# Optimization experiments

Measured on AMD Instinct MI355X. Metric: run time of the kernel, lower is better.

Reference implementation:

```python
import jax, jax.numpy as jnp
import numpy as np

MAX_DISP = 192

def _conv(x, w, b=None, stride=1, pad=0):
    y = jax.lax.conv_general_dilated(x, w, (stride, stride), [(pad, pad), (pad, pad)],
                                     dimension_numbers=('NCHW', 'OIHW', 'NCHW'))
    return y if b is None else y + b[None, :, None, None]

def _inorm(x):  # InstanceNorm2d, affine=False
    m = x.mean((2, 3), keepdims=True)
    v = x.var((2, 3), keepdims=True)
    return (x - m) * jax.lax.rsqrt(v + 1e-5)

def _bnorm(x):  # BatchNorm2d at init (gamma=1, beta=0), batch stats
    m = x.mean((0, 2, 3), keepdims=True)
    v = x.var((0, 2, 3), keepdims=True)
    return (x - m) * jax.lax.rsqrt(v + 1e-5)

def _encoder(x, w1, b1, w2, b2, w3, b3, norm):
    # simplified BasicEncoder: two stride-2 convs -> 1/4 resolution, then 1x1 proj
    x = jax.nn.relu(norm(_conv(x, w1, b1, 2, 3)))
    x = jax.nn.relu(norm(_conv(x, w2, b2, 2, 1)))
    return _conv(x, w3, b3, 1, 0)

def _forward(image1, image2, fnet_w1, fnet_b1, fnet_w2, fnet_b2, fnet_w3, fnet_b3,
             cnet_w1, cnet_b1, cnet_w2, cnet_b2, cnet_w3, cnet_b3,
             bform_a, bform_b, bform_cd_w, bform_cd_b,
             gru_wz, gru_bz, gru_wr, gru_br, gru_wq, gru_bq,
             disp_w1, disp_b1, disp_w2, disp_b2):
    i1 = 2.0 * (image1 / 255.0) - 1.0
    i2 = 2.0 * (image2 / 255.0) - 1.0
    fmap1 = _encoder(i1, fnet_w1, fnet_b1, fnet_w2, fnet_b2, fnet_w3, fnet_b3, _inorm)
    fmap2 = _encoder(i2, fnet_w1, fnet_b1, fnet_w2, fnet_b2, fnet_w3, fnet_b3, _inorm)
    hidden = jnp.tanh(_encoder(i1, cnet_w1, cnet_b1, cnet_w2, cnet_b2, cnet_w3, cnet_b3, _bnorm))
    Wf = fmap1.shape[3]
    for d in range(MAX_DISP // 4):  # 48 sequential width-sweep steps, shrinking overlap
        f1 = fmap1[:, :, :, d:]
        f2 = fmap2[:, :, :, :Wf - d] if d > 0 else fmap2
        # BilinearForm: a(x) + b(y) + cd(x*y), all 1x1 convs
        feat = _conv(f1, bform_a) + _conv(f2, bform_b) + _conv(f1 * f2, bform_cd_w, bform_cd_b)
        h = hidden[:, :, :, d:]
        # gru_input = cat(h, feat); ConvGRU cats hidden again -> [h, h, feat] = 96 ch
        hx = jnp.concatenate([h, h, feat], axis=1)
        z = jax.nn.sigmoid(_conv(hx, gru_wz, gru_bz, 1, 1))
        r = jax.nn.sigmoid(_conv(hx, gru_wr, gru_br, 1, 1))
        q = jnp.tanh(_conv(jnp.concatenate([r * h, h, feat], axis=1), gru_wq, gru_bq, 1, 1))
        h = (1.0 - z) * h + z * q
        hidden = hidden.at[:, :, :, d:].set(h)  # in-place scatter back
    # DisparityHead: conv3x3 -> relu -> conv3x3, negated
    return -_conv(jax.nn.relu(_conv(hidden, disp_w1, disp_b1, 1, 1)), disp_w2, disp_b2, 1, 1)

def setup_inputs():
    key = jax.random.key(0)
    ks = jax.random.split(key, 16)
    B, H, W, D = 1, 384, 640, 32
    def n(k, shape, scale=0.05):
        return (jax.random.normal(k, shape) * scale).astype(jnp.float32)
    z = lambda c: jnp.zeros((c,), jnp.float32)
    return {
        'image1': jax.random.uniform(ks[0], (B, 3, H, W), jnp.float32) * 255.0,
        'image2': jax.random.uniform(ks[1], (B, 3, H, W), jnp.float32) * 255.0,
        'fnet_w1': n(ks[2], (D, 3, 7, 7)), 'fnet_b1': z(D),
        'fnet_w2': n(ks[3], (D, D, 3, 3)), 'fnet_b2': z(D),
        'fnet_w3': n(ks[4], (D, D, 1, 1)), 'fnet_b3': z(D),
        'cnet_w1': n(ks[5], (D, 3, 7, 7)), 'cnet_b1': z(D),
        'cnet_w2': n(ks[6], (D, D, 3, 3)), 'cnet_b2': z(D),
        'cnet_w3': n(ks[7], (D, D, 1, 1)), 'cnet_b3': z(D),
        'bform_a': n(ks[8], (D, D, 1, 1)), 'bform_b': n(ks[9], (D, D, 1, 1)),
        'bform_cd_w': n(ks[10], (D, D, 1, 1)), 'bform_cd_b': z(D),
        'gru_wz': n(ks[11], (D, 3 * D, 3, 3)), 'gru_bz': z(D),
        'gru_wr': n(ks[12], (D, 3 * D, 3, 3)), 'gru_br': z(D),
        'gru_wq': n(ks[13], (D, 3 * D, 3, 3)), 'gru_bq': z(D),
        'disp_w1': n(ks[14], (64, D, 3, 3)), 'disp_b1': z(64),
        'disp_w2': n(ks[15], (1, 64, 3, 3)), 'disp_b2': z(1),
    }

def reference(image1, image2, fnet_w1, fnet_b1, fnet_w2, fnet_b2, fnet_w3, fnet_b3,
              cnet_w1, cnet_b1, cnet_w2, cnet_b2, cnet_w3, cnet_b3,
              bform_a, bform_b, bform_cd_w, bform_cd_b,
              gru_wz, gru_bz, gru_wr, gru_br, gru_wq, gru_bq,
              disp_w1, disp_b1, disp_w2, disp_b2):
    return _forward(image1, image2, fnet_w1, fnet_b1, fnet_w2, fnet_b2, fnet_w3, fnet_b3,
                    cnet_w1, cnet_b1, cnet_w2, cnet_b2, cnet_w3, cnet_b3,
                    bform_a, bform_b, bform_cd_w, bform_cd_b,
                    gru_wz, gru_bz, gru_wr, gru_br, gru_wq, gru_bq,
                    disp_w1, disp_b1, disp_w2, disp_b2)
```

## Files before the change

### kernel.cpp

```cpp
#include <hip/hip_runtime.h>
#include <math.h>

#define H0 384
#define W0 640
#define H1 192
#define W1 320
#define H2 96
#define W2 160
#define NP1 (H1*W1)
#define NP2 (H2*W2)
#define ND  48
#define NBLK2 (NP2/256)
#define CHW ((size_t)32*NP2)
#define PW 162
#define PH 98
#define PSL (PH*PW)
#define PCHW ((size_t)32*PSL)

typedef float v2f __attribute__((ext_vector_type(2)));


__global__ void zero_buf_kernel(float* __restrict__ p, size_t n) {
    size_t i = (size_t)blockIdx.x*256 + threadIdx.x;
    size_t stride = (size_t)gridDim.x*256;
    for (; i < n; i += stride) p[i] = 0.f;
}

__device__ __forceinline__ void twr_dev(const float* __restrict__ in, float* __restrict__ out,
                                        int idx, int CI, int K, int CO) {
    int co = idx % CO;
    int t  = idx / CO;
    int k  = t % K;
    int ci = t / K;
    out[idx] = in[(co*CI + ci)*K + k];
}

__global__ void prep_all(const float* __restrict__ fnet_w1, const float* __restrict__ cnet_w1,
                         const float* __restrict__ fnet_w2, const float* __restrict__ cnet_w2,
                         const float* __restrict__ fnet_w3, const float* __restrict__ cnet_w3,
                         const float* __restrict__ bform_a, const float* __restrict__ bform_b,
                         const float* __restrict__ bform_cd_w, const float* __restrict__ disp_w1,
                         const float* __restrict__ gru_wz, const float* __restrict__ gru_wr,
                         const float* __restrict__ gru_wq,
                         float* __restrict__ we1f, float* __restrict__ we1c,
                         float* __restrict__ we2f, float* __restrict__ we2c,
                         float* __restrict__ w3f, float* __restrict__ w3c,
                         float* __restrict__ wat, float* __restrict__ wbt,
                         float* __restrict__ wct, float* __restrict__ wd1t,
                         float4* __restrict__ wzrpk, float2* __restrict__ wqpk,
                         float* __restrict__ stats) {
    int i = blockIdx.x*256 + threadIdx.x;
    if (i < 4704) { twr_dev(fnet_w1, we1f, i, 3, 49, 32); return; }
    i -= 4704;
    if (i < 4704) { twr_dev(cnet_w1, we1c, i, 3, 49, 32); return; }
    i -= 4704;
    if (i < 9216) { twr_dev(fnet_w2, we2f, i, 32, 9, 32); return; }
    i -= 9216;
    if (i < 9216) { twr_dev(cnet_w2, we2c, i, 32, 9, 32); return; }
    i -= 9216;
    if (i < 1024) { twr_dev(fnet_w3, w3f, i, 32, 1, 32); return; }
    i -= 1024;
    if (i < 1024) { twr_dev(cnet_w3, w3c, i, 32, 1, 32); return; }
    i -= 1024;
    if (i < 1024) { twr_dev(bform_a, wat, i, 32, 1, 32); return; }
    i -= 1024;
    if (i < 1024) { twr_dev(bform_b, wbt, i, 32, 1, 32); return; }
    i -= 1024;
    if (i < 1024) { twr_dev(bform_cd_w, wct, i, 32, 1, 32); return; }
    i -= 1024;
    if (i < 18432) { twr_dev(disp_w1, wd1t, i, 32, 9, 64); return; }
    i -= 18432;
    if (i < 9216) {
        int k  = i % 9;
        int ci = (i/9) % 64;
        int cg = i / (9*64);
        int co0 = cg*2, co1 = co0 + 1;
        float z0, z1, r0, r1;
        if (ci < 32) {
            z0 = gru_wz[(co0*96 + ci)*9 + k] + gru_wz[(co0*96 + ci + 32)*9 + k];
            z1 = gru_wz[(co1*96 + ci)*9 + k] + gru_wz[(co1*96 + ci + 32)*9 + k];
            r0 = gru_wr[(co0*96 + ci)*9 + k] + gru_wr[(co0*96 + ci + 32)*9 + k];
            r1 = gru_wr[(co1*96 + ci)*9 + k] + gru_wr[(co1*96 + ci + 32)*9 + k];
        } else {
            z0 = gru_wz[(co0*96 + ci + 32)*9 + k];
            z1 = gru_wz[(co1*96 + ci + 32)*9 + k];
            r0 = gru_wr[(co0*96 + ci + 32)*9 + k];
            r1 = gru_wr[(co1*96 + ci + 32)*9 + k];
        }
        wzrpk[i] = make_float4(z0, z1, r0, r1);
        return;
    }
    i -= 9216;
    if (i < 13824) {
        int k  = i % 9;
        int ci = (i/9) % 96;
        int cg = i / (9*96);
        wqpk[i] = make_float2(gru_wq[((cg*2)*96 + ci)*9 + k], gru_wq[((cg*2+1)*96 + ci)*9 + k]);
        return;
    }
    i -= 13824;
    if (i < 384) stats[i] = 0.f;
}

__global__ void pad_init_kernel(const float* __restrict__ hidden, float* __restrict__ hwork) {
    int idx = blockIdx.x*256 + threadIdx.x;
    if (idx >= 32*PSL) return;
    int c = idx / PSL;
    int r = idx % PSL;
    int py = r / PW, px = r % PW;
    int y = py - 1, x = px - 1;
    float v = 0.f;
    if ((unsigned)y < (unsigned)H2 && (unsigned)x < (unsigned)W2)
        v = hidden[c*NP2 + y*W2 + x];
    hwork[idx] = v;
}


__global__ void conv7s2_v3(const float* __restrict__ img, const float* __restrict__ wt,
                           const float* __restrict__ b, float* __restrict__ out) {
    int cg = blockIdx.y;
    int co16 = cg*16;
    int sp = blockIdx.x*256 + threadIdx.x;
    int oy = sp / W1, ox = sp % W1;
    float acc[16];
    #pragma unroll
    for (int j = 0; j < 16; ++j) acc[j] = b[co16+j];
    for (int ci = 0; ci < 3; ++ci) {
        for (int ky = 0; ky < 7; ++ky) {
            int iy = 2*oy - 3 + ky;
            if ((unsigned)iy >= (unsigned)H0) continue;
            const float* row  = img + ci*(H0*W0) + iy*W0;
            const float* wrow = wt + (ci*49 + ky*7)*32 + co16;
            #pragma unroll
            for (int kx = 0; kx < 7; ++kx) {
                int ix = 2*ox - 3 + kx;
                if ((unsigned)ix >= (unsigned)W0) continue;
                float v = row[ix]*(2.0f/255.0f) - 1.0f;
                const float4* wp = (const float4*)(wrow + kx*32);
                #pragma unroll
                for (int j4 = 0; j4 < 4; ++j4) {
                    float4 w4 = wp[j4];
                    acc[4*j4+0] += v*w4.x; acc[4*j4+1] += v*w4.y;
                    acc[4*j4+2] += v*w4.z; acc[4*j4+3] += v*w4.w;
                }
            }
        }
    }
    #pragma unroll
    for (int j = 0; j < 16; ++j) out[(co16+j)*NP1 + sp] = acc[j];
}

__global__ void stats_partial_kernel(const float* __restrict__ x, int N, float* __restrict__ st) {
    int c = blockIdx.x >> 3, sl = blockIdx.x & 7;
    int chunk = N >> 3;
    const float4* p = (const float4*)(x + (size_t)c*N + (size_t)sl*chunk);
    int n4 = chunk >> 2;
    float s = 0.f, s2 = 0.f;
    for (int i = threadIdx.x; i < n4; i += 256) {
        float4 v = p[i];
        s  += v.x + v.y + v.z + v.w;
        s2 += v.x*v.x + v.y*v.y + v.z*v.z + v.w*v.w;
    }
    __shared__ float sh1[256], sh2[256];
    sh1[threadIdx.x] = s; sh2[threadIdx.x] = s2;
    __syncthreads();
    for (int o = 128; o > 0; o >>= 1) {
        if (threadIdx.x < o) { sh1[threadIdx.x] += sh1[threadIdx.x+o]; sh2[threadIdx.x] += sh2[threadIdx.x+o]; }
        __syncthreads();
    }
    if (threadIdx.x == 0) { atomicAdd(&st[2*c], sh1[0]); atomicAdd(&st[2*c+1], sh2[0]); }
}

__global__ void norm_relu_v2(float* __restrict__ x, const float* __restrict__ st, int N) {
    int c = blockIdx.y;
    float m    = st[2*c] / (float)N;
    float var  = st[2*c+1] / (float)N - m*m;
    float rstd = rsqrtf(var + 1e-5f);
    float4* p = (float4*)(x + (size_t)c*N);
    int i = blockIdx.x*256 + threadIdx.x;
    float4 v = p[i];
    v.x = fmaxf((v.x-m)*rstd, 0.f); v.y = fmaxf((v.y-m)*rstd, 0.f);
    v.z = fmaxf((v.z-m)*rstd, 0.f); v.w = fmaxf((v.w-m)*rstd, 0.f);
    p[i] = v;
}

__global__ void conv3s2_v2(const float* __restrict__ in, const float* __restrict__ wt,
                           const float* __restrict__ b, float* __restrict__ out) {
    int cg = blockIdx.x / (NP2/256);
    int sp = (blockIdx.x % (NP2/256))*256 + threadIdx.x;
    int co8 = cg*8;
    int oy = sp / W2, ox = sp % W2;
    float acc[8];
    #pragma unroll
    for (int j = 0; j < 8; ++j) acc[j] = b[co8+j];
    for (int ci = 0; ci < 32; ++ci) {
        const float* ip  = in + ci*NP1;
        const float* wci = wt + ci*9*32 + co8;
        #pragma unroll
        for (int ky = 0; ky < 3; ++ky) {
            int iy = 2*oy - 1 + ky;
            if ((unsigned)iy >= (unsigned)H1) continue;
            const float* row = ip + iy*W1;
            #pragma unroll
            for (int kx = 0; kx < 3; ++kx) {
                int ix = 2*ox - 1 + kx;
                if ((unsigned)ix >= (unsigned)W1) continue;
                float v = row[ix];
                const float4* wp = (const float4*)(wci + (ky*3+kx)*32);
                float4 w0 = wp[0], w1 = wp[1];
                acc[0] += v*w0.x; acc[1] += v*w0.y; acc[2] += v*w0.z; acc[3] += v*w0.w;
                acc[4] += v*w1.x; acc[5] += v*w1.y; acc[6] += v*w1.z; acc[7] += v*w1.w;
            }
        }
    }
    #pragma unroll
    for (int j = 0; j < 8; ++j) out[(co8+j)*NP2 + sp] = acc[j];
}

__global__ void conv1x1_v2(const float* __restrict__ in, const float* __restrict__ wt,
                           const float* __restrict__ b, float* __restrict__ out, int mode) {
    int cg = blockIdx.x / (NP2/256);
    int sp = (blockIdx.x % (NP2/256))*256 + threadIdx.x;
    int co8 = cg*8;
    float acc[8];
    #pragma unroll
    for (int j = 0; j < 8; ++j) acc[j] = b[co8+j];
    for (int ci = 0; ci < 32; ++ci) {
        float v = in[ci*NP2 + sp];
        const float4* wp = (const float4*)(wt + ci*32 + co8);
        float4 w0 = wp[0], w1 = wp[1];
        acc[0] += v*w0.x; acc[1] += v*w0.y; acc[2] += v*w0.z; acc[3] += v*w0.w;
        acc[4] += v*w1.x; acc[5] += v*w1.y; acc[6] += v*w1.z; acc[7] += v*w1.w;
    }
    #pragma unroll
    for (int j = 0; j < 8; ++j) {
        float a = acc[j];
        if (mode) a = tanhf(a);
        out[(co8+j)*NP2 + sp] = a;
    }
}


__global__ void feat0_pad_kernel(const float* __restrict__ fmap1, const float* __restrict__ fmap2,
                                 const float* __restrict__ wat, const float* __restrict__ wbt,
                                 const float* __restrict__ wct, const float* __restrict__ bc,
                                 float* __restrict__ featA) {
    int cg  = blockIdx.x / NBLK2;
    int sp  = (blockIdx.x % NBLK2)*256 + threadIdx.x;
    int y = sp / W2;
    int gx = sp % W2;
    int co8 = cg*8;
    float acc[8];
    #pragma unroll
    for (int j = 0; j < 8; ++j) acc[j] = bc[co8+j];
    for (int ci = 0; ci < 32; ++ci) {
        float f1 = fmap1[ci*NP2 + sp];
        float f2 = fmap2[ci*NP2 + sp];
        float f12 = f1*f2;
        const float4* ap = (const float4*)(wat + ci*32 + co8);
        const float4* bp = (const float4*)(wbt + ci*32 + co8);
        const float4* cp = (const float4*)(wct + ci*32 + co8);
        float4 a0 = ap[0], a1 = ap[1];
        float4 b0 = bp[0], b1 = bp[1];
        float4 c0 = cp[0], c1 = cp[1];
        acc[0] += f1*a0.x + f2*b0.x + f12*c0.x;
        acc[1] += f1*a0.y + f2*b0.y + f12*c0.y;
        acc[2] += f1*a0.z + f2*b0.z + f12*c0.z;
        acc[3] += f1*a0.w + f2*b0.w + f12*c0.w;
        acc[4] += f1*a1.x + f2*b1.x + f12*c1.x;
        acc[5] += f1*a1.y + f2*b1.y + f12*c1.y;
        acc[6] += f1*a1.z + f2*b1.z + f12*c1.z;
        acc[7] += f1*a1.w + f2*b1.w + f12*c1.w;
    }
    float* dst = featA + (size_t)(y+1)*PW + (gx+1);
    #pragma unroll
    for (int j = 0; j < 8; ++j) dst[(size_t)(co8+j)*PSL] = acc[j];
}


__global__ __launch_bounds__(256, 4)
void zrf_v6(const float* __restrict__ hworkA, const float* __restrict__ featA,
            const float* __restrict__ fmap1, const float* __restrict__ fmap2,
            const float4* __restrict__ wzrpk,
            const float* __restrict__ wat, const float* __restrict__ wbt,
            const float* __restrict__ wct, const float* __restrict__ bfc,
            const float* __restrict__ bz, const float* __restrict__ br,
            float* __restrict__ zbuf, float* __restrict__ rhpad,
            float* __restrict__ featB, int d, int Wd) {
    __shared__ v2f lwz[64*9], lwr[64*9];
    __shared__ v2f lfa[32], lfb[32], lfc[32];
    int cg  = blockIdx.y;
    int co0 = cg*2;
    {
        const float4* wsrc = wzrpk + (size_t)cg*576;
        for (int i = threadIdx.x; i < 576; i += 256) {
            float4 w = wsrc[i];
            lwz[i] = (v2f){w.x, w.y};
            lwr[i] = (v2f){w.z, w.w};
        }
        if (threadIdx.x < 32) {
            int ci = threadIdx.x;
            lfa[ci] = (v2f){wat[ci*32+co0], wat[ci*32+co0+1]};
            lfb[ci] = (v2f){wbt[ci*32+co0], wbt[ci*32+co0+1]};
            lfc[ci] = (v2f){wct[ci*32+co0], wct[ci*32+co0+1]};
        }
    }
    __syncthreads();
    int sp2 = blockIdx.x*256 + threadIdx.x;
    if (sp2 >= 48*Wd) return;
    int rp = sp2 / Wd;
    int lx = sp2 - rp*Wd;
    int y0 = rp*2;
    int gx = d + lx;
    size_t poff = (size_t)(y0+1)*PW + (gx+1);

    if (lx == 0) {
        #pragma unroll
        for (int j = 0; j < 2; ++j) {
            rhpad[(size_t)(co0+j)*PSL + poff - 1]      = 0.f;
            rhpad[(size_t)(co0+j)*PSL + poff + PW - 1] = 0.f;
        }
    }

    int dn = d + 1;
    if (dn < ND) {
        if (lx == 0) {
            #pragma unroll
            for (int j = 0; j < 2; ++j) {
                featB[(size_t)(co0+j)*PSL + poff]      = 0.f;
                featB[(size_t)(co0+j)*PSL + poff + PW] = 0.f;
            }
        } else {
            v2f f0 = (v2f){bfc[co0], bfc[co0+1]};
            v2f f1 = f0;
            int base1 = y0*W2 + gx;
            #pragma unroll 2
            for (int ci = 0; ci < 32; ++ci) {
                float a1 = fmap1[ci*NP2 + base1];
                float a2 = fmap1[ci*NP2 + base1 + W2];
                float b1 = fmap2[ci*NP2 + base1 - dn];
                float b2 = fmap2[ci*NP2 + base1 + W2 - dn];
                v2f wa = lfa[ci], wb = lfb[ci], wc = lfc[ci];
                f0 += wa*(v2f){a1,a1} + wb*(v2f){b1,b1} + wc*(v2f){a1*b1,a1*b1};
                f1 += wa*(v2f){a2,a2} + wb*(v2f){b2,b2} + wc*(v2f){a2*b2,a2*b2};
            }
            featB[(size_t)co0*PSL + poff]          = f0.x;
            featB[(size_t)(co0+1)*PSL + poff]      = f0.y;
            featB[(size_t)co0*PSL + poff + PW]     = f1.x;
            featB[(size_t)(co0+1)*PSL + poff + PW] = f1.y;
        }
    }

    v2f az0 = (v2f){bz[co0], bz[co0+1]}, az1 = az0;
    v2f ar0 = (v2f){br[co0], br[co0+1]}, ar1 = ar0;
    #pragma unroll
    for (int pass = 0; pass < 2; ++pass) {
        const float* p = (pass == 0 ? hworkA : featA) + poff;
        const v2f* wz = lwz + pass*288;
        const v2f* wr = lwr + pass*288;
        #pragma unroll 2
        for (int ci = 0; ci < 32; ++ci) {
            float v[12];
            #pragma unroll
            for (int r = 0; r < 4; ++r) {
                v[r*3+0] = p[(r-1)*PW - 1];
                v[r*3+1] = p[(r-1)*PW    ];
                v[r*3+2] = p[(r-1)*PW + 1];
            }
            #pragma unroll
            for (int k = 0; k < 9; ++k) {
                int ky = k/3, kx = k - 3*ky;
                float t0 = v[ky*3+kx];
                float t1 = v[(ky+1)*3+kx];
                v2f wzk = wz[k], wrk = wr[k];
                az0 += wzk*(v2f){t0,t0}; az1 += wzk*(v2f){t1,t1};
                ar0 += wrk*(v2f){t0,t0}; ar1 += wrk*(v2f){t1,t1};
            }
            p += PSL;
            wz += 9; wr += 9;
        }
    }
    v2f z0, z1, r0, r1;
    z0.x = 1.f/(1.f + __expf(-az0.x)); z0.y = 1.f/(1.f + __expf(-az0.y));
    z1.x = 1.f/(1.f + __expf(-az1.x)); z1.y = 1.f/(1.f + __expf(-az1.y));
    r0.x = 1.f/(1.f + __expf(-ar0.x)); r0.y = 1.f/(1.f + __expf(-ar0.y));
    r1.x = 1.f/(1.f + __expf(-ar1.x)); r1.y = 1.f/(1.f + __expf(-ar1.y));
    int ub = y0*W2 + gx;
    float h00 = hworkA[(size_t)co0*PSL + poff];
    float h01 = hworkA[(size_t)(co0+1)*PSL + poff];
    float h10 = hworkA[(size_t)co0*PSL + poff + PW];
    float h11 = hworkA[(size_t)(co0+1)*PSL + poff + PW];
    zbuf[(size_t)co0*NP2 + ub]          = z0.x;
    zbuf[(size_t)(co0+1)*NP2 + ub]      = z0.y;
    zbuf[(size_t)co0*NP2 + ub + W2]     = z1.x;
    zbuf[(size_t)(co0+1)*NP2 + ub + W2] = z1.y;
    rhpad[(size_t)co0*PSL + poff]          = r0.x*h00;
    rhpad[(size_t)(co0+1)*PSL + poff]      = r0.y*h01;
    rhpad[(size_t)co0*PSL + poff + PW]     = r1.x*h10;
    rhpad[(size_t)(co0+1)*PSL + poff + PW] = r1.y*h11;
}

__global__ __launch_bounds__(256, 4)
void qup_v6(const float* __restrict__ rhpad, const float* __restrict__ hworkA,
            const float* __restrict__ featA, const float* __restrict__ zbuf,
            const float2* __restrict__ qpk, const float* __restrict__ bq,
            float* __restrict__ hfinal, float* __restrict__ hworkB, int d, int Wd) {
    __shared__ v2f lw[96*9];
    int cg  = blockIdx.y;
    int co0 = cg*2;
    {
        const float2* wsrc = qpk + (size_t)cg*864;
        for (int i = threadIdx.x; i < 864; i += 256) {
            float2 w = wsrc[i];
            lw[i] = (v2f){w.x, w.y};
        }
    }
    __syncthreads();
    int sp2 = blockIdx.x*256 + threadIdx.x;
    if (sp2 >= 48*Wd) return;
    int rp = sp2 / Wd;
    int lx = sp2 - rp*Wd;
    int y0 = rp*2;
    int gx = d + lx;
    size_t poff = (size_t)(y0+1)*PW + (gx+1);

    v2f a0 = (v2f){bq[co0], bq[co0+1]};
    v2f a1 = a0;
    #pragma unroll
    for (int pass = 0; pass < 3; ++pass) {
        const float* p = (pass == 0 ? rhpad : (pass == 1 ? hworkA : featA)) + poff;
        const v2f* wp = lw + pass*288;
        #pragma unroll 2
        for (int ci = 0; ci < 32; ++ci) {
            float v[12];
            #pragma unroll
            for (int r = 0; r < 4; ++r) {
                v[r*3+0] = p[(r-1)*PW - 1];
                v[r*3+1] = p[(r-1)*PW    ];
                v[r*3+2] = p[(r-1)*PW + 1];
            }
            #pragma unroll
            for (int k = 0; k < 9; ++k) {
                int ky = k/3, kx = k - 3*ky;
                float t0 = v[ky*3+kx];
                float t1 = v[(ky+1)*3+kx];
                v2f wk = wp[k];
                a0 += wk*(v2f){t0,t0};
                a1 += wk*(v2f){t1,t1};
            }
            p += PSL;
            wp += 9;
        }
    }
    float q00 = tanhf(a0.x), q01 = tanhf(a0.y);
    float q10 = tanhf(a1.x), q11 = tanhf(a1.y);
    int ub = y0*W2 + gx;
    #pragma unroll
    for (int j = 0; j < 2; ++j) {
        float qa = (j == 0) ? q00 : q01;
        float qb = (j == 0) ? q10 : q11;
        size_t pidx = (size_t)(co0+j)*PSL + poff;
        size_t uidx = (size_t)(co0+j)*NP2 + ub;
        float z_a = zbuf[uidx];
        float z_b = zbuf[uidx + W2];
        float h_a = hworkA[pidx];
        float h_b = hworkA[pidx + PW];
        float hn_a = (1.f - z_a)*h_a + z_a*qa;
        float hn_b = (1.f - z_b)*h_b + z_b*qb;
        hfinal[pidx]      = hn_a;
        hfinal[pidx + PW] = hn_b;
        hworkB[pidx]      = (lx == 0) ? 0.f : hn_a;
        hworkB[pidx + PW] = (lx == 0) ? 0.f : hn_b;
    }
}


__global__ __launch_bounds__(256, 4)
void disp1_v6(const float* __restrict__ hfinal, const float* __restrict__ wt,
              const float* __restrict__ b, float* __restrict__ out) {
    __shared__ float4 lw[288];
    int cg  = blockIdx.y;
    int co0 = cg*4;
    for (int i = threadIdx.x; i < 288; i += 256)
        lw[i] = *(const float4*)&wt[i*64 + co0];
    __syncthreads();
    int sp2 = blockIdx.x*256 + threadIdx.x;
    int y0 = (sp2 / W2)*2;
    int gx = sp2 % W2;
    size_t poff = (size_t)(y0+1)*PW + (gx+1);
    float4 bb = *(const float4*)&b[co0];
    float acc0[4] = {bb.x, bb.y, bb.z, bb.w};
    float acc1[4] = {bb.x, bb.y, bb.z, bb.w};
    const float* p = hfinal + poff;
    #pragma unroll 2
    for (int ci = 0; ci < 32; ++ci) {
        float v[12];
        #pragma unroll
        for (int r = 0; r < 4; ++r) {
            v[r*3+0] = p[(r-1)*PW - 1];
            v[r*3+1] = p[(r-1)*PW    ];
            v[r*3+2] = p[(r-1)*PW + 1];
        }
        #pragma unroll
        for (int k = 0; k < 9; ++k) {
            int ky = k/3, kx = k - 3*ky;
            float t0 = v[ky*3+kx];
            float t1 = v[(ky+1)*3+kx];
            float4 w = lw[ci*9+k];
            acc0[0] += t0*w.x; acc0[1] += t0*w.y; acc0[2] += t0*w.z; acc0[3] += t0*w.w;
            acc1[0] += t1*w.x; acc1[1] += t1*w.y; acc1[2] += t1*w.z; acc1[3] += t1*w.w;
        }
        p += PSL;
    }
    int ub = y0*W2 + gx;
    #pragma unroll
    for (int j = 0; j < 4; ++j) {
        out[(co0+j)*NP2 + ub]      = fmaxf(acc0[j], 0.f);
        out[(co0+j)*NP2 + ub + W2] = fmaxf(acc1[j], 0.f);
    }
}

__global__ void disp2_part_kernel(const float* __restrict__ in, const float* __restrict__ w,
                                  float* __restrict__ part) {
    __shared__ float lw[8*9];
    int g  = blockIdx.x / NBLK2;
    int sp = (blockIdx.x % NBLK2)*256 + threadIdx.x;
    if (threadIdx.x < 72) lw[threadIdx.x] = w[g*72 + threadIdx.x];
    __syncthreads();
    int y = sp / W2, x = sp % W2;
    float acc = 0.f;
    #pragma unroll
    for (int ci = 0; ci < 8; ++ci) {
        const float* ip = in + (g*8 + ci)*NP2;
        #pragma unroll
        for (int dy = 0; dy < 3; ++dy) {
            int ys = y+dy-1; if ((unsigned)ys >= (unsigned)H2) continue;
            const float* row = ip + ys*W2;
            #pragma unroll
            for (int dx = 0; dx < 3; ++dx) {
                int xs = x+dx-1; if ((unsigned)xs >= (unsigned)W2) continue;
                acc += lw[ci*9+dy*3+dx] * row[xs];
            }
        }
    }
    part[g*NP2 + sp] = acc;
}

__global__ void disp2_comb_kernel(const float* __restrict__ part, const float* __restrict__ b,
                                  float* __restrict__ out) {
    int sp = blockIdx.x*256 + threadIdx.x;
    float acc = b[0];
    #pragma unroll
    for (int g = 0; g < 8; ++g) acc += part[g*NP2 + sp];
    out[sp] = -acc;
}


extern "C" void kernel_launch(void* const* d_in, const int* in_sizes, int n_in,
                              void* d_out, int out_size, void* d_ws, size_t ws_size,
                              hipStream_t stream) {
    const float* image1   = (const float*)d_in[0];
    const float* image2   = (const float*)d_in[1];
    const float* fnet_w1  = (const float*)d_in[2];
    const float* fnet_b1  = (const float*)d_in[3];
    const float* fnet_w2  = (const float*)d_in[4];
    const float* fnet_b2  = (const float*)d_in[5];
    const float* fnet_w3  = (const float*)d_in[6];
    const float* fnet_b3  = (const float*)d_in[7];
    const float* cnet_w1  = (const float*)d_in[8];
    const float* cnet_b1  = (const float*)d_in[9];
    const float* cnet_w2  = (const float*)d_in[10];
    const float* cnet_b2  = (const float*)d_in[11];
    const float* cnet_w3  = (const float*)d_in[12];
    const float* cnet_b3  = (const float*)d_in[13];
    const float* bform_a  = (const float*)d_in[14];
    const float* bform_b  = (const float*)d_in[15];
    const float* bform_cd_w = (const float*)d_in[16];
    const float* bform_cd_b = (const float*)d_in[17];
    const float* gru_wz   = (const float*)d_in[18];
    const float* gru_bz   = (const float*)d_in[19];
    const float* gru_wr   = (const float*)d_in[20];
    const float* gru_br   = (const float*)d_in[21];
    const float* gru_wq   = (const float*)d_in[22];
    const float* gru_bq   = (const float*)d_in[23];
    const float* disp_w1  = (const float*)d_in[24];
    const float* disp_b1  = (const float*)d_in[25];
    const float* disp_w2  = (const float*)d_in[26];
    const float* disp_b2  = (const float*)d_in[27];

    float* ws = (float*)d_ws;
    size_t o = 0;
    float* e1     = ws + o; o += (size_t)32*NP1;
    float* e2     = ws + o; o += CHW;
    float* fmap1  = ws + o; o += CHW;
    float* fmap2  = ws + o; o += CHW;
    float* hidden = ws + o; o += CHW;
    float* zbuf   = ws + o; o += CHW;
    float* hwork0 = ws + o; o += PCHW;
    float* hwork1 = ws + o; o += PCHW;
    float* rhpad  = ws + o; o += PCHW;
    float* feat0  = ws + o; o += PCHW;
    float* feat1  = ws + o; o += PCHW;
    float* hfinal = ws + o; o += PCHW;
    float* stats  = ws + o; o += 384;
    float* wzrpk  = ws + o; o += 16*64*9*4;
    float* wqpk   = ws + o; o += 16*96*9*2;
    float* we1f   = ws + o; o += 3*49*32;
    float* we1c   = ws + o; o += 3*49*32;
    float* we2f   = ws + o; o += 32*9*32;
    float* we2c   = ws + o; o += 32*9*32;
    float* w3f    = ws + o; o += 32*32;
    float* w3c    = ws + o; o += 32*32;
    float* wat    = ws + o; o += 32*32;
    float* wbt    = ws + o; o += 32*32;
    float* wct    = ws + o; o += 32*32;
    float* wd1t   = ws + o; o += 32*9*64;
    float* disp1buf  = e1;
    float* disp2part = e2;

    prep_all<<<(74816 + 255)/256, 256, 0, stream>>>(
        fnet_w1, cnet_w1, fnet_w2, cnet_w2, fnet_w3, cnet_w3,
        bform_a, bform_b, bform_cd_w, disp_w1, gru_wz, gru_wr, gru_wq,
        we1f, we1c, we2f, we2c, w3f, w3c, wat, wbt, wct, wd1t,
        (float4*)wzrpk, (float2*)wqpk, stats);

    auto encoder = [&](const float* img, const float* w1t, const float* b1,
                       const float* w2t, const float* b2,
                       const float* w3t, const float* b3, float* dst, int mode,
                       float* st1, float* st2) {
        conv7s2_v3<<<dim3(NP1/256, 2), 256, 0, stream>>>(img, w1t, b1, e1);
        stats_partial_kernel<<<256, 256, 0, stream>>>(e1, NP1, st1);
        norm_relu_v2<<<dim3(NP1/1024, 32), 256, 0, stream>>>(e1, st1, NP1);
        conv3s2_v2<<<4*(NP2/256), 256, 0, stream>>>(e1, w2t, b2, e2);
        stats_partial_kernel<<<256, 256, 0, stream>>>(e2, NP2, st2);
        norm_relu_v2<<<dim3(NP2/1024, 32), 256, 0, stream>>>(e2, st2, NP2);
        conv1x1_v2<<<4*(NP2/256), 256, 0, stream>>>(e2, w3t, b3, dst, mode);
    };
    encoder(image1, we1f, fnet_b1, we2f, fnet_b2, w3f, fnet_b3, fmap1, 0, stats+0,   stats+64);
    encoder(image2, we1f, fnet_b1, we2f, fnet_b2, w3f, fnet_b3, fmap2, 0, stats+128, stats+192);
    encoder(image1, we1c, cnet_b1, we2c, cnet_b2, w3c, cnet_b3, hidden, 1, stats+256, stats+320);

    zero_buf_kernel<<<2048, 256, 0, stream>>>(hwork1, 5*PCHW);
    pad_init_kernel<<<(32*PSL+255)/256, 256, 0, stream>>>(hidden, hwork0);
    feat0_pad_kernel<<<4*NBLK2, 256, 0, stream>>>(fmap1, fmap2, wat, wbt, wct,
                                                  bform_cd_b, feat0);

    float* hwA = hwork0; float* hwB = hwork1;
    float* ftA = feat0;  float* ftB = feat1;
    for (int d = 0; d < ND; ++d) {
        int Wd = W2 - d;
        int nblk = (48*Wd + 255)/256;
        zrf_v6<<<dim3(nblk, 16), 256, 0, stream>>>(hwA, ftA, fmap1, fmap2,
                                                   (const float4*)wzrpk,
                                                   wat, wbt, wct, bform_cd_b,
                                                   gru_bz, gru_br, zbuf, rhpad, ftB, d, Wd);
        qup_v6<<<dim3(nblk, 16), 256, 0, stream>>>(rhpad, hwA, ftA, zbuf,
                                                   (const float2*)wqpk, gru_bq,
                                                   hfinal, hwB, d, Wd);
        float* t;
        t = hwA; hwA = hwB; hwB = t;
        t = ftA; ftA = ftB; ftB = t;
    }

    disp1_v6<<<dim3(30, 16), 256, 0, stream>>>(hfinal, wd1t, disp_b1, disp1buf);
    disp2_part_kernel<<<8*NBLK2, 256, 0, stream>>>(disp1buf, disp_w2, disp2part);
    disp2_comb_kernel<<<NBLK2, 256, 0, stream>>>(disp2part, disp_b2, (float*)d_out);
}
```

Baseline: 3.010 ms.

## Fuse encoder norm-relu into convs, share image1 first conv, skip redundant hfinal writes

Removes the standalone normalise+ReLU passes by computing the mean and rstd from the stats inside the following 3x3 and 1x1 convs and applying them on load. A dual 7x7 conv computes the fnet and cnet first layers for image1 in one pass over the image, using a separate buffer for each. In the GRU update kernel, hfinal is written only when a column leaves the overlap (lx==0) or on the last step, which cuts per-step global stores. The cost is repeated rsqrt per input channel in the fused convs and more register pressure in the dual conv.

```diff
diff --git a/kernel.cpp b/kernel.cpp
--- a/kernel.cpp
+++ b/kernel.cpp
@@ -116,6 +116,46 @@
 }
 
 
+__global__ __launch_bounds__(256, 4)
+void conv7s2_dual(const float* __restrict__ img,
+                  const float* __restrict__ wtf, const float* __restrict__ wtc,
+                  const float* __restrict__ bf, const float* __restrict__ bc,
+                  float* __restrict__ outf, float* __restrict__ outc) {
+    int co8 = blockIdx.y*8;
+    int sp = blockIdx.x*256 + threadIdx.x;
+    int oy = sp / W1, ox = sp % W1;
+    float af[8], ac[8];
+    #pragma unroll
+    for (int j = 0; j < 8; ++j) { af[j] = bf[co8+j]; ac[j] = bc[co8+j]; }
+    for (int ci = 0; ci < 3; ++ci) {
+        for (int ky = 0; ky < 7; ++ky) {
+            int iy = 2*oy - 3 + ky;
+            if ((unsigned)iy >= (unsigned)H0) continue;
+            const float* row  = img + ci*(H0*W0) + iy*W0;
+            int wbase = (ci*49 + ky*7)*32 + co8;
+            #pragma unroll
+            for (int kx = 0; kx < 7; ++kx) {
+                int ix = 2*ox - 3 + kx;
+                if ((unsigned)ix >= (unsigned)W0) continue;
+                float v = row[ix]*(2.0f/255.0f) - 1.0f;
+                const float4* wpf = (const float4*)(wtf + wbase + kx*32);
+                const float4* wpc = (const float4*)(wtc + wbase + kx*32);
+                float4 f0 = wpf[0], f1 = wpf[1];
+                float4 c0 = wpc[0], c1 = wpc[1];
+                af[0] += v*f0.x; af[1] += v*f0.y; af[2] += v*f0.z; af[3] += v*f0.w;
+                af[4] += v*f1.x; af[5] += v*f1.y; af[6] += v*f1.z; af[7] += v*f1.w;
+                ac[0] += v*c0.x; ac[1] += v*c0.y; ac[2] += v*c0.z; ac[3] += v*c0.w;
+                ac[4] += v*c1.x; ac[5] += v*c1.y; ac[6] += v*c1.z; ac[7] += v*c1.w;
+            }
+        }
+    }
+    #pragma unroll
+    for (int j = 0; j < 8; ++j) {
+        outf[(co8+j)*NP1 + sp] = af[j];
+        outc[(co8+j)*NP1 + sp] = ac[j];
+    }
+}
+
 __global__ void conv7s2_v3(const float* __restrict__ img, const float* __restrict__ wt,
                            const float* __restrict__ b, float* __restrict__ out) {
     int cg = blockIdx.y;
@@ -171,29 +211,20 @@
     if (threadIdx.x == 0) { atomicAdd(&st[2*c], sh1[0]); atomicAdd(&st[2*c+1], sh2[0]); }
 }
 
-__global__ void norm_relu_v2(float* __restrict__ x, const float* __restrict__ st, int N) {
-    int c = blockIdx.y;
-    float m    = st[2*c] / (float)N;
-    float var  = st[2*c+1] / (float)N - m*m;
-    float rstd = rsqrtf(var + 1e-5f);
-    float4* p = (float4*)(x + (size_t)c*N);
-    int i = blockIdx.x*256 + threadIdx.x;
-    float4 v = p[i];
-    v.x = fmaxf((v.x-m)*rstd, 0.f); v.y = fmaxf((v.y-m)*rstd, 0.f);
-    v.z = fmaxf((v.z-m)*rstd, 0.f); v.w = fmaxf((v.w-m)*rstd, 0.f);
-    p[i] = v;
-}
-
-__global__ void conv3s2_v2(const float* __restrict__ in, const float* __restrict__ wt,
-                           const float* __restrict__ b, float* __restrict__ out) {
-    int cg = blockIdx.x / (NP2/256);
-    int sp = (blockIdx.x % (NP2/256))*256 + threadIdx.x;
+__global__ void conv3s2_fused(const float* __restrict__ in, const float* __restrict__ st,
+                              const float* __restrict__ wt, const float* __restrict__ b,
+                              float* __restrict__ out) {
+    int cg = blockIdx.x / NBLK2;
+    int sp = (blockIdx.x % NBLK2)*256 + threadIdx.x;
     int co8 = cg*8;
     int oy = sp / W2, ox = sp % W2;
     float acc[8];
     #pragma unroll
     for (int j = 0; j < 8; ++j) acc[j] = b[co8+j];
     for (int ci = 0; ci < 32; ++ci) {
+        float m    = st[2*ci] * (1.0f/NP1);
+        float var  = st[2*ci+1] * (1.0f/NP1) - m*m;
+        float rstd = rsqrtf(var + 1e-5f);
         const float* ip  = in + ci*NP1;
         const float* wci = wt + ci*9*32 + co8;
         #pragma unroll
@@ -205,11 +236,11 @@
             for (int kx = 0; kx < 3; ++kx) {
                 int ix = 2*ox - 1 + kx;
                 if ((unsigned)ix >= (unsigned)W1) continue;
-                float v = row[ix];
+                float t = fmaxf((row[ix] - m)*rstd, 0.f);
                 const float4* wp = (const float4*)(wci + (ky*3+kx)*32);
                 float4 w0 = wp[0], w1 = wp[1];
-                acc[0] += v*w0.x; acc[1] += v*w0.y; acc[2] += v*w0.z; acc[3] += v*w0.w;
-                acc[4] += v*w1.x; acc[5] += v*w1.y; acc[6] += v*w1.z; acc[7] += v*w1.w;
+                acc[0] += t*w0.x; acc[1] += t*w0.y; acc[2] += t*w0.z; acc[3] += t*w0.w;
+                acc[4] += t*w1.x; acc[5] += t*w1.y; acc[6] += t*w1.z; acc[7] += t*w1.w;
             }
         }
     }
@@ -217,20 +248,24 @@
     for (int j = 0; j < 8; ++j) out[(co8+j)*NP2 + sp] = acc[j];
 }
 
-__global__ void conv1x1_v2(const float* __restrict__ in, const float* __restrict__ wt,
-                           const float* __restrict__ b, float* __restrict__ out, int mode) {
-    int cg = blockIdx.x / (NP2/256);
-    int sp = (blockIdx.x % (NP2/256))*256 + threadIdx.x;
+__global__ void conv1x1_fused(const float* __restrict__ in, const float* __restrict__ st,
+                              const float* __restrict__ wt, const float* __restrict__ b,
+                              float* __restrict__ out, int mode) {
+    int cg = blockIdx.x / NBLK2;
+    int sp = (blockIdx.x % NBLK2)*256 + threadIdx.x;
     int co8 = cg*8;
     float acc[8];
     #pragma unroll
     for (int j = 0; j < 8; ++j) acc[j] = b[co8+j];
     for (int ci = 0; ci < 32; ++ci) {
-        float v = in[ci*NP2 + sp];
+        float m    = st[2*ci] * (1.0f/NP2);
+        float var  = st[2*ci+1] * (1.0f/NP2) - m*m;
+        float rstd = rsqrtf(var + 1e-5f);
+        float t = fmaxf((in[ci*NP2 + sp] - m)*rstd, 0.f);
         const float4* wp = (const float4*)(wt + ci*32 + co8);
         float4 w0 = wp[0], w1 = wp[1];
-        acc[0] += v*w0.x; acc[1] += v*w0.y; acc[2] += v*w0.z; acc[3] += v*w0.w;
-        acc[4] += v*w1.x; acc[5] += v*w1.y; acc[6] += v*w1.z; acc[7] += v*w1.w;
+        acc[0] += t*w0.x; acc[1] += t*w0.y; acc[2] += t*w0.z; acc[3] += t*w0.w;
+        acc[4] += t*w1.x; acc[5] += t*w1.y; acc[6] += t*w1.z; acc[7] += t*w1.w;
     }
     #pragma unroll
     for (int j = 0; j < 8; ++j) {
@@ -467,8 +502,10 @@
         float h_b = hworkA[pidx + PW];
         float hn_a = (1.f - z_a)*h_a + z_a*qa;
         float hn_b = (1.f - z_b)*h_b + z_b*qb;
-        hfinal[pidx]      = hn_a;
-        hfinal[pidx + PW] = hn_b;
+        if (lx == 0 || d == ND-1) {
+            hfinal[pidx]      = hn_a;
+            hfinal[pidx + PW] = hn_b;
+        }
         hworkB[pidx]      = (lx == 0) ? 0.f : hn_a;
         hworkB[pidx + PW] = (lx == 0) ? 0.f : hn_b;
     }
@@ -590,7 +627,8 @@
 
     float* ws = (float*)d_ws;
     size_t o = 0;
-    float* e1     = ws + o; o += (size_t)32*NP1;
+    float* e1f    = ws + o; o += (size_t)32*NP1;
+    float* e1c    = ws + o; o += (size_t)32*NP1;
     float* e2     = ws + o; o += CHW;
     float* fmap1  = ws + o; o += CHW;
     float* fmap2  = ws + o; o += CHW;
@@ -615,8 +653,8 @@
     float* wbt    = ws + o; o += 32*32;
     float* wct    = ws + o; o += 32*32;
     float* wd1t   = ws + o; o += 32*9*64;
-    float* disp1buf  = e1;
-    float* disp2part = e2;
+    float* disp1buf  = e1f;
+    float* disp2part = e1c;
 
     prep_all<<<(74816 + 255)/256, 256, 0, stream>>>(
         fnet_w1, cnet_w1, fnet_w2, cnet_w2, fnet_w3, cnet_w3,
@@ -624,21 +662,21 @@
         we1f, we1c, we2f, we2c, w3f, w3c, wat, wbt, wct, wd1t,
         (float4*)wzrpk, (float2*)wqpk, stats);
 
-    auto encoder = [&](const float* img, const float* w1t, const float* b1,
-                       const float* w2t, const float* b2,
-                       const float* w3t, const float* b3, float* dst, int mode,
-                       float* st1, float* st2) {
-        conv7s2_v3<<<dim3(NP1/256, 2), 256, 0, stream>>>(img, w1t, b1, e1);
-        stats_partial_kernel<<<256, 256, 0, stream>>>(e1, NP1, st1);
-        norm_relu_v2<<<dim3(NP1/1024, 32), 256, 0, stream>>>(e1, st1, NP1);
-        conv3s2_v2<<<4*(NP2/256), 256, 0, stream>>>(e1, w2t, b2, e2);
-        stats_partial_kernel<<<256, 256, 0, stream>>>(e2, NP2, st2);
-        norm_relu_v2<<<dim3(NP2/1024, 32), 256, 0, stream>>>(e2, st2, NP2);
-        conv1x1_v2<<<4*(NP2/256), 256, 0, stream>>>(e2, w3t, b3, dst, mode);
-    };
-    encoder(image1, we1f, fnet_b1, we2f, fnet_b2, w3f, fnet_b3, fmap1, 0, stats+0,   stats+64);
-    encoder(image2, we1f, fnet_b1, we2f, fnet_b2, w3f, fnet_b3, fmap2, 0, stats+128, stats+192);
-    encoder(image1, we1c, cnet_b1, we2c, cnet_b2, w3c, cnet_b3, hidden, 1, stats+256, stats+320);
+    conv7s2_dual<<<dim3(NP1/256, 4), 256, 0, stream>>>(image1, we1f, we1c, fnet_b1, cnet_b1,
+                                                       e1f, e1c);
+    stats_partial_kernel<<<256, 256, 0, stream>>>(e1f, NP1, stats+0);
+    stats_partial_kernel<<<256, 256, 0, stream>>>(e1c, NP1, stats+64);
+    conv3s2_fused<<<4*NBLK2, 256, 0, stream>>>(e1f, stats+0, we2f, fnet_b2, e2);
+    stats_partial_kernel<<<256, 256, 0, stream>>>(e2, NP2, stats+128);
+    conv1x1_fused<<<4*NBLK2, 256, 0, stream>>>(e2, stats+128, w3f, fnet_b3, fmap1, 0);
+    conv3s2_fused<<<4*NBLK2, 256, 0, stream>>>(e1c, stats+64, we2c, cnet_b2, e2);
+    stats_partial_kernel<<<256, 256, 0, stream>>>(e2, NP2, stats+192);
+    conv1x1_fused<<<4*NBLK2, 256, 0, stream>>>(e2, stats+192, w3c, cnet_b3, hidden, 1);
+    conv7s2_v3<<<dim3(NP1/256, 2), 256, 0, stream>>>(image2, we1f, fnet_b1, e1f);
+    stats_partial_kernel<<<256, 256, 0, stream>>>(e1f, NP1, stats+256);
+    conv3s2_fused<<<4*NBLK2, 256, 0, stream>>>(e1f, stats+256, we2f, fnet_b2, e2);
+    stats_partial_kernel<<<256, 256, 0, stream>>>(e2, NP2, stats+320);
+    conv1x1_fused<<<4*NBLK2, 256, 0, stream>>>(e2, stats+320, w3f, fnet_b3, fmap2, 0);
 
     zero_buf_kernel<<<2048, 256, 0, stream>>>(hwork1, 5*PCHW);
     pad_init_kernel<<<(32*PSL+255)/256, 256, 0, stream>>>(hidden, hwork0);
```

Result: no change. 2.965 ms (-1.5%).
